# Kernel optimization log

Measured on AMD Instinct MI355X. Metric: run time of the kernel, lower is better.

The kernel has to match this reference:

```python
import jax, jax.numpy as jnp
import numpy as np

T, N, H, G = 4, 100000, 128, 1024
LN2 = float(np.log(2.0))
EPS = 1e-5


def ssp(x):
    # shifted softplus: softplus(x) - softplus(0)
    return jax.nn.softplus(x) - LN2


def layernorm(x, g, b):
    m = jnp.mean(x, axis=-1, keepdims=True)
    v = jnp.var(x, axis=-1, keepdims=True)
    return (x - m) * jax.lax.rsqrt(v + EPS) * g + b


def mlp3(x, Ws, bs, gs, bts):
    # 3 stacked Linear -> LayerNorm -> SSP stages
    for i in range(3):
        x = ssp(layernorm(x @ Ws[i] + bs[i], gs[i], bts[i]))
    return x


def setup_inputs() -> dict:
    key = jax.random.key(0)
    ks = jax.random.split(key, 8)
    s = 1.0 / np.sqrt(H)
    batch = jnp.sort((jnp.arange(N, dtype=jnp.int64) * G) // N).astype(jnp.int32)
    return {
        "x_proc": jax.random.normal(ks[0], (T, N, H), jnp.float32),
        "x_enc": jax.random.normal(ks[1], (N, H), jnp.float32),
        "batch": batch,
        "pW": jax.random.normal(ks[2], (3, H, H), jnp.float32) * s,
        "pb": jnp.zeros((3, H), jnp.float32),
        "pg": jnp.ones((3, H), jnp.float32),
        "pbt": jnp.zeros((3, H), jnp.float32),
        "eW": jax.random.normal(ks[3], (3, H, H), jnp.float32) * s,
        "eb": jnp.zeros((3, H), jnp.float32),
        "eg": jnp.ones((3, H), jnp.float32),
        "ebt": jnp.zeros((3, H), jnp.float32),
        "wp": jax.random.normal(ks[4], (H, 1), jnp.float32) * s,
        "bp": jnp.zeros((1,), jnp.float32),
        "we": jax.random.normal(ks[5], (H, 1), jnp.float32) * s,
        "be": jnp.zeros((1,), jnp.float32),
    }


def reference(x_proc, x_enc, batch, pW, pb, pg, pbt, eW, eb, eg, ebt, wp, bp, we, be):
    h_proc = mlp3(x_proc, pW, pb, pg, pbt)          # [T, N, H]
    h_enc = mlp3(x_enc, eW, eb, eg, ebt)            # [N, H]
    seg = lambda z: jax.ops.segment_sum(z, batch, num_segments=G)
    pooled_proc = jax.vmap(seg)(h_proc)             # [T, G, H]
    pooled_enc = seg(h_enc)                         # [G, H]
    target = pooled_proc @ wp + bp + (pooled_enc @ we + be)[None]  # [T, G, 1]
    return target.reshape(-1, G)                    # [T, G]
```

## Files before the change

### kernel.cpp

```cpp
#include <hip/hip_runtime.h>
#include <hip/hip_bf16.h>

typedef unsigned short u16;
typedef unsigned int u32;
typedef __bf16 bf16x8 __attribute__((ext_vector_type(8)));
typedef float f32x16 __attribute__((ext_vector_type(16)));
typedef float f32x4 __attribute__((ext_vector_type(4)));
typedef float f32x2 __attribute__((ext_vector_type(2)));
typedef u32 u32x4 __attribute__((ext_vector_type(4)));

typedef struct { f32x2 h[2]; } f32x4p;
typedef struct { f32x2 h[8]; } f32x16p;

typedef __attribute__((address_space(1))) const u32 glb_u32;
typedef __attribute__((address_space(3))) u32 lds_u32;

#define NN 100000
#define NPROC_BLOCKS 3125
#define NENC_BLOCKS 782
#define LN2F 0.69314718055994530942f
#define LOG2EF 1.44269504088896340736f
#define CSTRIDE 1284

__device__ __forceinline__ u16 f2bf(float f) {
  u32 u = __float_as_uint(f);
  u32 r = u + 0x7fffu + ((u >> 16) & 1u);
  return (u16)(r >> 16);
}

__device__ __forceinline__ u32 pk2(float a, float b) {
  float2 f2; f2.x = a; f2.y = b;
  __hip_bfloat162 h = __float22bfloat162_rn(f2);
  u32 r;
  __builtin_memcpy(&r, &h, 4);
  return r;
}

__device__ __forceinline__ float l2p1e(float xp) {
  return __builtin_amdgcn_logf(1.0f + __builtin_amdgcn_exp2f(xp));
}

__global__ void prep_kernel(const float* __restrict__ pW, const float* __restrict__ eW,
                            const float* __restrict__ pb, const float* __restrict__ pg,
                            const float* __restrict__ pbt,
                            const float* __restrict__ eb, const float* __restrict__ eg,
                            const float* __restrict__ ebt,
                            const float* __restrict__ wp, const float* __restrict__ we,
                            const float* __restrict__ bp, const float* __restrict__ be,
                            u16* __restrict__ wt, float* __restrict__ cprep,
                            float* __restrict__ out) {
  int bx = blockIdx.x;
  int t = threadIdx.x;
  if (bx < 384) {
    int idx = bx * 256 + t;
    int m = idx >> 14;
    int within = idx & 16383;
    int r = within >> 7;
    int c = within & 127;
    int k = (((c >> 3) ^ (r & 15)) << 3) | (c & 7);
    const float* src = (m < 3) ? pW : eW;
    int ms = (m < 3) ? m : m - 3;
    float w = src[ms * 16384 + k * 128 + r];
    if (ms >= 1) w *= LN2F;
    wt[idx] = f2bf(w);
    if (idx < 4096) out[idx] = bp[0] + be[0];
  } else {
    int net = bx - 384;
    const float* W  = net ? eW : pW;
    const float* b  = net ? eb : pb;
    const float* g  = net ? eg : pg;
    const float* bt = net ? ebt : pbt;
    const float* wv = net ? we : wp;
    float* cp = cprep + net * CSTRIDE;
    if (t < 128) {
      int j = t;
      #pragma unroll
      for (int s = 0; s < 3; ++s) {
        float bb = b[s * 128 + j];
        if (s >= 1) {
          float cs = 0.f;
          #pragma unroll 8
          for (int k = 0; k < 128; ++k) cs += W[s * 16384 + k * 128 + j];
          bb -= LN2F * cs;
        }
        cp[(s * 3 + 0) * 128 + j] = bb;
        cp[(s * 3 + 1) * 128 + j] = g[s * 128 + j] * LOG2EF;
        cp[(s * 3 + 2) * 128 + j] = bt[s * 128 + j] * LOG2EF;
      }
      cp[9 * 128 + j] = LN2F * wv[j];
    }
    if (t == 0) {
      float ssum = 0.f;
      #pragma unroll 8
      for (int j = 0; j < 128; ++j) ssum += wv[j];
      cp[1280] = -LN2F * ssum;
    }
  }
}

__global__ __launch_bounds__(256, 3)
void mlp_kernel(const float* __restrict__ x_proc, const float* __restrict__ x_enc,
                const u16* __restrict__ wt, const float* __restrict__ cprep,
                const int* __restrict__ batch, float* __restrict__ out) {
  __shared__ __align__(16) unsigned char wbuf[32768];
  __shared__ f32x4 cball[10][32];
  __shared__ float c0s;

  const bool is_proc = blockIdx.x < NPROC_BLOCKS;
  const int bid2 = is_proc ? blockIdx.x : blockIdx.x - NPROC_BLOCKS;
  const float* x = is_proc ? x_proc : x_enc;
  const unsigned char* wgb = (const unsigned char*)(is_proc ? wt : wt + 49152);
  const float* cp = cprep + (is_proc ? 0 : CSTRIDE);
  const int nrows = is_proc ? 400000 : 100000;

  const int tid = threadIdx.x;
  const int lane = tid & 63;
  const int wid = tid >> 6;
  const int l31 = lane & 31;
  const u32 hi = (u32)(lane >> 5);
  const int brow = bid2 * 128;

  auto issue_w = [&](int s_) {
    #pragma unroll
    for (int i = 0; i < 8; ++i) {
      const unsigned char* gp = wgb + s_ * 32768 + i * 4096 + tid * 16;
      unsigned char* lp = wbuf + i * 4096 + wid * 1024;
      __builtin_amdgcn_global_load_lds((const glb_u32*)(const void*)gp,
                                       (lds_u32*)(void*)lp, 16, 0, 0);
    }
  };

  issue_w(0);

  for (int i = tid; i < 320; i += 256)
    ((f32x4*)cball)[i] = *(const f32x4*)(cp + i * 4);
  if (tid == 0) c0s = cp[1280];

  const int rloc = wid * 32 + l31;
  const int grow = brow + rloc;
  const float* xr = x + (size_t)((grow < nrows) ? grow : (nrows - 1)) * 128 + (int)hi * 8;
  bf16x8 bfr[8];
  {
    f32x4 a[16];
    #pragma unroll
    for (int ks = 0; ks < 8; ++ks) {
      a[2 * ks]     = *(const f32x4*)(xr + ks * 16);
      a[2 * ks + 1] = *(const f32x4*)(xr + ks * 16 + 4);
    }
    #pragma unroll
    for (int ks = 0; ks < 8; ++ks) {
      u32x4 tq;
      tq.x = pk2(a[2 * ks][0], a[2 * ks][1]);
      tq.y = pk2(a[2 * ks][2], a[2 * ks][3]);
      tq.z = pk2(a[2 * ks + 1][0], a[2 * ks + 1][1]);
      tq.w = pk2(a[2 * ks + 1][2], a[2 * ks + 1][3]);
      bfr[ks] = __builtin_bit_cast(bf16x8, tq);
    }
  }

  float pfin = 0.0f;

  #pragma unroll
  for (int s = 0; s < 3; ++s) {
    __syncthreads();

    f32x16 acc[4];
    #pragma unroll
    for (int jf = 0; jf < 4; ++jf)
      #pragma unroll
      for (int q = 0; q < 4; ++q) {
        f32x4 b4 = cball[s * 3 + 0][jf * 8 + 2 * q + (int)hi];
        acc[jf][4 * q + 0] = b4[0];
        acc[jf][4 * q + 1] = b4[1];
        acc[jf][4 * q + 2] = b4[2];
        acc[jf][4 * q + 3] = b4[3];
      }

    #pragma unroll
    for (int ks = 0; ks < 8; ++ks) {
      int aoff = l31 * 256 + (((2 * ks + (int)hi) ^ (l31 & 15)) << 4);
      #pragma unroll
      for (int jf = 0; jf < 4; ++jf) {
        const bf16x8 afrag = *(const bf16x8*)(const void*)(wbuf + jf * 8192 + aoff);
        acc[jf] = __builtin_amdgcn_mfma_f32_32x32x16_bf16(afrag, bfr[ks], acc[jf], 0, 0, 0);
      }
      if (ks & 1) __builtin_amdgcn_sched_barrier(0);
    }

    if (s < 2) {
      __syncthreads();
      issue_w(s + 1);
    }

    f32x2 s1v = {0.f, 0.f}, s2v = {0.f, 0.f};
    #pragma unroll
    for (int jf = 0; jf < 4; ++jf) {
      f32x16p az = __builtin_bit_cast(f32x16p, acc[jf]);
      f32x2 p1 = {0.f, 0.f}, p2 = {0.f, 0.f};
      #pragma unroll
      for (int e = 0; e < 8; ++e) {
        f32x2 v = az.h[e];
        p1 += v;
        p2 = __builtin_elementwise_fma(v, v, p2);
      }
      s1v += p1; s2v += p2;
    }
    float s1 = s1v[0] + s1v[1];
    float s2 = s2v[0] + s2v[1];
    s1 += __shfl_xor(s1, 32, 64);
    s2 += __shfl_xor(s2, 32, 64);
    float mean = s1 * 0.0078125f;
    float var = s2 * 0.0078125f - mean * mean;
    float rstd = rsqrtf(var + 1e-5f);
    float nmr = -mean * rstd;
    const f32x2 rstd2 = {rstd, rstd};
    const f32x2 nmr2 = {nmr, nmr};

    if (s < 2) {
      #pragma unroll
      for (int ks = 0; ks < 8; ++ks) {
        int jf = ks >> 1, q0 = (ks & 1) << 1;
        f32x16p az = __builtin_bit_cast(f32x16p, acc[jf]);
        uint2 wq[2];
        #pragma unroll
        for (int qq = 0; qq < 2; ++qq) {
          int q = q0 + qq;
          f32x4p g = __builtin_bit_cast(f32x4p, cball[s * 3 + 1][jf * 8 + 2 * q + (int)hi]);
          f32x4p t = __builtin_bit_cast(f32x4p, cball[s * 3 + 2][jf * 8 + 2 * q + (int)hi]);
          f32x2 u0 = __builtin_elementwise_fma(az.h[2 * q + 0], rstd2, nmr2);
          f32x2 u1 = __builtin_elementwise_fma(az.h[2 * q + 1], rstd2, nmr2);
          f32x2 x0 = __builtin_elementwise_fma(u0, g.h[0], t.h[0]);
          f32x2 x1 = __builtin_elementwise_fma(u1, g.h[1], t.h[1]);
          wq[qq].x = pk2(l2p1e(x0[0]), l2p1e(x0[1]));
          wq[qq].y = pk2(l2p1e(x1[0]), l2p1e(x1[1]));
        }
        u32 sx = hi ? wq[0].x : wq[1].x;
        u32 sy = hi ? wq[0].y : wq[1].y;
        u32 rx = (u32)__shfl_xor((int)sx, 32, 64);
        u32 ry = (u32)__shfl_xor((int)sy, 32, 64);
        u32x4 tq;
        tq.x = hi ? rx : wq[0].x;
        tq.y = hi ? ry : wq[0].y;
        tq.z = hi ? wq[1].x : rx;
        tq.w = hi ? wq[1].y : ry;
        bfr[ks] = __builtin_bit_cast(bf16x8, tq);
      }
    } else {
      float pa = 0.f, pb2 = 0.f;
      #pragma unroll
      for (int jf = 0; jf < 4; ++jf) {
        f32x16p az = __builtin_bit_cast(f32x16p, acc[jf]);
        #pragma unroll
        for (int q = 0; q < 4; ++q) {
          f32x4 g4 = cball[7][jf * 8 + 2 * q + (int)hi];
          f32x4 t4 = cball[8][jf * 8 + 2 * q + (int)hi];
          f32x4 w4 = cball[9][jf * 8 + 2 * q + (int)hi];
          f32x4p g = __builtin_bit_cast(f32x4p, g4);
          f32x4p t = __builtin_bit_cast(f32x4p, t4);
          f32x2 u0 = __builtin_elementwise_fma(az.h[2 * q + 0], rstd2, nmr2);
          f32x2 u1 = __builtin_elementwise_fma(az.h[2 * q + 1], rstd2, nmr2);
          f32x2 x0 = __builtin_elementwise_fma(u0, g.h[0], t.h[0]);
          f32x2 x1 = __builtin_elementwise_fma(u1, g.h[1], t.h[1]);
          pa = __builtin_fmaf(l2p1e(x0[0]), w4[0], pa);
          pb2 = __builtin_fmaf(l2p1e(x0[1]), w4[1], pb2);
          pa = __builtin_fmaf(l2p1e(x1[0]), w4[2], pa);
          pb2 = __builtin_fmaf(l2p1e(x1[1]), w4[3], pb2);
        }
      }
      pfin = pa + pb2;
    }
  }

  pfin += __shfl_xor(pfin, 32, 64);
  if (grow < nrows) {
    pfin += c0s;
    int cell;
    if (is_proc) {
      int tt = grow / NN;
      cell = tt * 1024 + batch[grow - tt * NN];
    } else {
      cell = batch[grow];
    }
    int ca = __shfl(cell, 0, 32);
    int cz = __shfl(cell, 31, 32);
    if (ca == cz) {
      float r = pfin;
      #pragma unroll
      for (int off = 1; off < 32; off <<= 1) r += __shfl_xor(r, off, 64);
      if (hi == 0) {
        if (is_proc) {
          if (l31 == 0) atomicAdd(out + ca, r);
        } else {
          if (l31 < 4) atomicAdd(out + l31 * 1024 + ca, r);
        }
      }
    } else if (hi == 0) {
      if (is_proc) {
        atomicAdd(out + cell, pfin);
      } else {
        #pragma unroll
        for (int t2 = 0; t2 < 4; ++t2) atomicAdd(out + t2 * 1024 + cell, pfin);
      }
    }
  }
}

extern "C" void kernel_launch(void* const* d_in, const int* in_sizes, int n_in,
                              void* d_out, int out_size, void* d_ws, size_t ws_size,
                              hipStream_t stream) {
  const float* x_proc = (const float*)d_in[0];
  const float* x_enc  = (const float*)d_in[1];
  const int*   batch  = (const int*)d_in[2];
  const float* pW  = (const float*)d_in[3];
  const float* pb  = (const float*)d_in[4];
  const float* pg  = (const float*)d_in[5];
  const float* pbt = (const float*)d_in[6];
  const float* eW  = (const float*)d_in[7];
  const float* eb  = (const float*)d_in[8];
  const float* eg  = (const float*)d_in[9];
  const float* ebt = (const float*)d_in[10];
  const float* wp  = (const float*)d_in[11];
  const float* bp  = (const float*)d_in[12];
  const float* we  = (const float*)d_in[13];
  const float* be  = (const float*)d_in[14];

  float* out = (float*)d_out;
  u16* wt_ws = (u16*)d_ws;
  float* cprep = (float*)((char*)d_ws + 196608);

  prep_kernel<<<386, 256, 0, stream>>>(pW, eW, pb, pg, pbt, eb, eg, ebt,
                                       wp, we, bp, be, wt_ws, cprep, out);
  mlp_kernel<<<NPROC_BLOCKS + NENC_BLOCKS, 256, 0, stream>>>(
      x_proc, x_enc, wt_ws, cprep, batch, out);
}
```

Measured before the change: 137.2 us.

## Parallelize prep column sums across blocks and loosen MFMA sched barriers

The prep kernel's per-net constant computation is split from two blocks into six, one per (net, layer) pair. Each layer's column sum over W is also split across two thread halves and combined through shared memory, and the wv reduction now uses a wave shuffle instead of a serial loop. This shortens the serial tail of the small prep launch that precedes the main MLP kernel. In the main kernel, the scheduling barrier in the MFMA loop now fires every four k-steps instead of every two, giving the compiler more freedom to interleave LDS loads with MFMAs, at some risk of higher register pressure.

Result: slower. 142.4 us (+3.8%).

```diff
diff --git a/kernel.cpp b/kernel.cpp
--- a/kernel.cpp
+++ b/kernel.cpp
@@ -65,35 +65,45 @@
     wt[idx] = f2bf(w);
     if (idx < 4096) out[idx] = bp[0] + be[0];
   } else {
-    int net = bx - 384;
+    int which = bx - 384;
+    int net = which / 3;
+    int s = which % 3;
     const float* W  = net ? eW : pW;
     const float* b  = net ? eb : pb;
     const float* g  = net ? eg : pg;
     const float* bt = net ? ebt : pbt;
     const float* wv = net ? we : wp;
     float* cp = cprep + net * CSTRIDE;
+    __shared__ float red[128];
+
+    int j = t & 127;
+    int half = t >> 7;
     if (t < 128) {
-      int j = t;
-      #pragma unroll
-      for (int s = 0; s < 3; ++s) {
-        float bb = b[s * 128 + j];
-        if (s >= 1) {
-          float cs = 0.f;
-          #pragma unroll 8
-          for (int k = 0; k < 128; ++k) cs += W[s * 16384 + k * 128 + j];
-          bb -= LN2F * cs;
-        }
-        cp[(s * 3 + 0) * 128 + j] = bb;
-        cp[(s * 3 + 1) * 128 + j] = g[s * 128 + j] * LOG2EF;
-        cp[(s * 3 + 2) * 128 + j] = bt[s * 128 + j] * LOG2EF;
-      }
-      cp[9 * 128 + j] = LN2F * wv[j];
-    }
-    if (t == 0) {
-      float ssum = 0.f;
+      cp[(s * 3 + 1) * 128 + j] = g[s * 128 + j] * LOG2EF;
+      cp[(s * 3 + 2) * 128 + j] = bt[s * 128 + j] * LOG2EF;
+    }
+    if (s == 0) {
+      if (t < 128) {
+        cp[0 * 128 + j] = b[j];
+        cp[9 * 128 + j] = LN2F * wv[j];
+      }
+      if (t < 64) {
+        float v = wv[t] + wv[t + 64];
+        #pragma unroll
+        for (int off = 1; off < 64; off <<= 1) v += __shfl_xor(v, off, 64);
+        if (t == 0) cp[1280] = -LN2F * v;
+      }
+    } else {
+      float part = 0.f;
+      const float* Ws = W + s * 16384 + half * 64 * 128 + j;
       #pragma unroll 8
-      for (int j = 0; j < 128; ++j) ssum += wv[j];
-      cp[1280] = -LN2F * ssum;
+      for (int k = 0; k < 64; ++k) part += Ws[k * 128];
+      if (half == 1) red[j] = part;
+      __syncthreads();
+      if (half == 0) {
+        float cs = part + red[j];
+        cp[(s * 3 + 0) * 128 + j] = b[s * 128 + j] - LN2F * cs;
+      }
     }
   }
 }
@@ -184,7 +194,7 @@
         const bf16x8 afrag = *(const bf16x8*)(const void*)(wbuf + jf * 8192 + aoff);
         acc[jf] = __builtin_amdgcn_mfma_f32_32x32x16_bf16(afrag, bfr[ks], acc[jf], 0, 0, 0);
       }
-      if (ks & 1) __builtin_amdgcn_sched_barrier(0);
+      if ((ks & 3) == 3) __builtin_amdgcn_sched_barrier(0);
     }
 
     if (s < 2) {
@@ -328,7 +338,7 @@
   u16* wt_ws = (u16*)d_ws;
   float* cprep = (float*)((char*)d_ws + 196608);
 
-  prep_kernel<<<386, 256, 0, stream>>>(pW, eW, pb, pg, pbt, eb, eg, ebt,
+  prep_kernel<<<390, 256, 0, stream>>>(pW, eW, pb, pg, pbt, eb, eg, ebt,
                                        wp, we, bp, be, wt_ws, cprep, out);
   mlp_kernel<<<NPROC_BLOCKS + NENC_BLOCKS, 256, 0, stream>>>(
       x_proc, x_enc, wt_ws, cprep, batch, out);
```
